# Optimization experiments

Measured on AMD Instinct MI355X. Metric: run time of the kernel, lower is better.

Reference implementation:

```python
import jax, jax.numpy as jnp
import numpy as np
import math

EPS = 1e-5

def layernorm(x, g, b):
    mu = jnp.mean(x, axis=-1, keepdims=True)
    var = jnp.var(x, axis=-1, keepdims=True)
    return (x - mu) * jax.lax.rsqrt(var + EPS) * g + b

def setup_inputs() -> dict:
    key = jax.random.key(0)
    ks = jax.random.split(key, 12)
    B, T, E, H = 4, 2048, 128, 8
    D = H * E          # 1024
    F = 4 * D          # 4096
    s = 0.02
    return {
        "X":     jax.random.normal(ks[0], (B, T, E), jnp.float32),
        "ln1_g": jnp.ones((E,), jnp.float32),
        "ln1_b": jnp.zeros((E,), jnp.float32),
        "Wq":    jax.random.normal(ks[1], (H, E, E), jnp.float32) * s,
        "bq":    jax.random.normal(ks[2], (H, E), jnp.float32) * s,
        "Wk":    jax.random.normal(ks[3], (H, E, E), jnp.float32) * s,
        "bk":    jax.random.normal(ks[4], (H, E), jnp.float32) * s,
        "Wv":    jax.random.normal(ks[5], (H, E, E), jnp.float32) * s,
        "bv":    jax.random.normal(ks[6], (H, E), jnp.float32) * s,
        "ln2_g": jnp.ones((D,), jnp.float32),
        "ln2_b": jnp.zeros((D,), jnp.float32),
        "W1":    jax.random.normal(ks[7], (D, F), jnp.float32) * s,
        "b1":    jax.random.normal(ks[8], (F,), jnp.float32) * s,
        "W2":    jax.random.normal(ks[9], (F, E), jnp.float32) * s,
        "b2":    jax.random.normal(ks[10], (E,), jnp.float32) * s,
    }

def reference(X, ln1_g, ln1_b, Wq, bq, Wk, bk, Wv, bv, ln2_g, ln2_b, W1, b1, W2, b2):
    B, T, E = X.shape
    Xn = layernorm(X, ln1_g, ln1_b)                       # [B,T,E]
    # per-head projections, vectorized over heads
    q = jnp.einsum('bte,hef->bhtf', Xn, Wq) + bq[None, :, None, :]
    k = jnp.einsum('bte,hef->bhtf', Xn, Wk) + bk[None, :, None, :]
    v = jnp.einsum('bte,hef->bhtf', Xn, Wv) + bv[None, :, None, :]
    scores = jnp.einsum('bhtf,bhsf->bhts', q, k) / math.sqrt(E)
    # causal mask: positions with s > t set to -inf (triu offset=1)
    t_idx = jnp.arange(T)
    mask = t_idx[None, :] > t_idx[:, None]                # [T,S], True above diag
    scores = jnp.where(mask[None, None], -jnp.inf, scores)
    # NOTE: original code softmaxes over dim = ndim-2, i.e. the QUERY axis
    attn = jax.nn.softmax(scores, axis=-2)
    out = jnp.einsum('bhts,bhsf->bhtf', attn, v)          # [B,H,T,E]
    # concat heads along last dim (head order preserved)
    concat = jnp.transpose(out, (0, 2, 1, 3)).reshape(B, T, -1)  # [B,T,H*E]
    h = layernorm(concat, ln2_g, ln2_b)
    mid = jax.nn.gelu(h @ W1 + b1, approximate=False)
    return mid @ W2 + b2                                   # [B,T,E]
```

## Files before the change

kernel.cpp:

```cpp
#include <hip/hip_runtime.h>
#include <hip/hip_bf16.h>
#include <math.h>

typedef __hip_bfloat16 bf16;
typedef __attribute__((ext_vector_type(8))) short short8;
typedef __attribute__((ext_vector_type(4))) float floatx4;

#define B_ 4
#define T_ 2048
#define E_ 128
#define H_ 8
#define D_ 1024
#define F_ 4096
#define M_ 8192

static __device__ __forceinline__ float b2f(bf16 v){ return __bfloat162float(v); }
static __device__ __forceinline__ bf16  f2b(float v){ return __float2bfloat16(v); }
static __device__ __forceinline__ short f2bs(float v){ bf16 h = __float2bfloat16(v); return *(short*)&h; }

static __device__ __forceinline__ void glds16(const bf16* g, void* l){
  __builtin_amdgcn_global_load_lds((const __attribute__((address_space(1))) void*)g,
                                   (__attribute__((address_space(3))) void*)l, 16, 0, 0);
}

__global__ void detect_dtype_k(const unsigned int* __restrict__ g, int* __restrict__ flag){
  if (threadIdx.x == 0) flag[0] = (g[0] == 0x3F803F80u) ? 1 : 0;
}

__global__ void convert_misc_k(const void* s0, const void* s1, const void* s2, const void* s3,
                               const void* s4, const void* s5, const void* s6, const void* s7,
                               const void* s8,
                               bf16* g1, bf16* b1, bf16* bqkv, bf16* g2, bf16* b2l,
                               bf16* bb1, bf16* bb2, const int* __restrict__ flag){
  int i = blockIdx.x * 256 + threadIdx.x;
  if (i >= 9600) return;
  int fl = flag[0];
  const void* src; bf16* dst; int off;
  if      (i <  128){ src = s0; dst = g1;          off = i;        }
  else if (i <  256){ src = s1; dst = b1;          off = i - 128;  }
  else if (i < 1280){ src = s2; dst = bqkv;        off = i - 256;  }
  else if (i < 2304){ src = s3; dst = bqkv + 1024; off = i - 1280; }
  else if (i < 3328){ src = s4; dst = bqkv + 2048; off = i - 2304; }
  else if (i < 4352){ src = s5; dst = g2;          off = i - 3328; }
  else if (i < 5376){ src = s6; dst = b2l;         off = i - 4352; }
  else if (i < 9472){ src = s7; dst = bb1;         off = i - 5376; }
  else              { src = s8; dst = bb2;         off = i - 9472; }
  dst[off] = fl ? ((const bf16*)src)[off] : f2b(((const float*)src)[off]);
}

__global__ __launch_bounds__(256) void transpose_cvt_k(const void* __restrict__ src, bf16* __restrict__ dst,
                                                       int R, int C, const int* __restrict__ flag){
  __shared__ float tile[32][33];
  int r0 = blockIdx.y * 32, c0 = blockIdx.x * 32;
  int tx = threadIdx.x & 31, ty = threadIdx.x >> 5;
  int fl = flag[0];
  #pragma unroll
  for (int i = 0; i < 32; i += 8){
    size_t idx = (size_t)(r0 + ty + i) * C + c0 + tx;
    tile[ty + i][tx] = fl ? b2f(((const bf16*)src)[idx]) : ((const float*)src)[idx];
  }
  __syncthreads();
  #pragma unroll
  for (int i = 0; i < 32; i += 8){
    dst[(size_t)(c0 + ty + i) * R + r0 + tx] = f2b(tile[tx][ty + i]);
  }
}

__global__ __launch_bounds__(256) void transpose_qkv_k(const void* __restrict__ Wq, const void* __restrict__ Wk,
                                                       const void* __restrict__ Wv, bf16* __restrict__ dst,
                                                       const int* __restrict__ flag){
  __shared__ float tile[32][33];
  int sel = blockIdx.z >> 3, h = blockIdx.z & 7;
  const void* src = (sel == 0) ? Wq : (sel == 1) ? Wk : Wv;
  size_t mo = (size_t)h * E_ * E_;
  bf16* d = dst + (size_t)sel * H_ * E_ * E_ + mo;
  int r0 = blockIdx.y * 32, c0 = blockIdx.x * 32;
  int tx = threadIdx.x & 31, ty = threadIdx.x >> 5;
  int fl = flag[0];
  #pragma unroll
  for (int i = 0; i < 32; i += 8){
    size_t idx = mo + (size_t)(r0 + ty + i) * E_ + c0 + tx;
    tile[ty + i][tx] = fl ? b2f(((const bf16*)src)[idx]) : ((const float*)src)[idx];
  }
  __syncthreads();
  #pragma unroll
  for (int i = 0; i < 32; i += 8){
    d[(size_t)(c0 + ty + i) * E_ + r0 + tx] = f2b(tile[tx][ty + i]);
  }
}

__global__ __launch_bounds__(256) void ln1_k(const void* __restrict__ X, const bf16* __restrict__ g,
                                             const bf16* __restrict__ b, bf16* __restrict__ out,
                                             const int* __restrict__ flag){
  int row = blockIdx.x * 4 + (threadIdx.x >> 6);
  int lane = threadIdx.x & 63;
  float x0, x1;
  if (flag[0]){
    const bf16* xp = (const bf16*)X + (size_t)row * E_;
    x0 = b2f(xp[lane]); x1 = b2f(xp[lane + 64]);
  } else {
    const float* xp = (const float*)X + (size_t)row * E_;
    x0 = xp[lane]; x1 = xp[lane + 64];
  }
  float s  = x0 + x1;
  float s2 = x0 * x0 + x1 * x1;
  #pragma unroll
  for (int o = 32; o > 0; o >>= 1){ s += __shfl_xor(s, o, 64); s2 += __shfl_xor(s2, o, 64); }
  float mu  = s * (1.0f / 128.0f);
  float var = s2 * (1.0f / 128.0f) - mu * mu;
  float rs  = rsqrtf(var + 1e-5f);
  out[(size_t)row * E_ + lane]      = f2b((x0 - mu) * rs * b2f(g[lane])      + b2f(b[lane]));
  out[(size_t)row * E_ + lane + 64] = f2b((x1 - mu) * rs * b2f(g[lane + 64]) + b2f(b[lane + 64]));
}

template<int EPI>
__global__ __launch_bounds__(256, 3) void gemm_mfma_k(
    const bf16* __restrict__ A, const bf16* __restrict__ Bt,
    const bf16* __restrict__ bias, void* __restrict__ out,
    int K, const int* __restrict__ flag)
{
  __shared__ __align__(16) short As[2][4][128][8];
  __shared__ __align__(16) short Bs[2][4][128][8];
  int tid = threadIdx.x;
  int lane = tid & 63, w = tid >> 6;
  int quad = lane >> 4, l16 = lane & 15;
  int wm = w & 1, wn = w >> 1;
  int m0 = blockIdx.y * 128;
  int n0, nit;
  size_t kstart;
  if (EPI == 3){ n0 = 0; int kc = K >> 3; kstart = (size_t)blockIdx.x * kc; nit = kc >> 5; }
  else         { n0 = blockIdx.x * 128; kstart = 0; nit = K >> 5; }

  int seg0 = w * 2, seg1 = w * 2 + 1;
  int kq0 = seg0 & 3, mb0 = (seg0 >> 2) * 64;
  int kq1 = seg1 & 3, mb1 = (seg1 >> 2) * 64;
  const bf16* pa0 = A  + (size_t)(m0 + mb0 + lane) * K + kstart + kq0 * 8;
  const bf16* pa1 = A  + (size_t)(m0 + mb1 + lane) * K + kstart + kq1 * 8;
  const bf16* pb0 = Bt + (size_t)(n0 + mb0 + lane) * K + kstart + kq0 * 8;
  const bf16* pb1 = Bt + (size_t)(n0 + mb1 + lane) * K + kstart + kq1 * 8;
  uint4 ra0 = *(const uint4*)pa0, ra1 = *(const uint4*)pa1;
  uint4 rb0 = *(const uint4*)pb0, rb1 = *(const uint4*)pb1;

  floatx4 acc[4][4];
  #pragma unroll
  for (int i = 0; i < 4; i++)
    #pragma unroll
    for (int j = 0; j < 4; j++) acc[i][j] = (floatx4){0.f, 0.f, 0.f, 0.f};

  for (int it = 0; it < nit; it++){
    int buf = it & 1;
    *(uint4*)&As[buf][kq0][mb0 + lane][0] = ra0;
    *(uint4*)&As[buf][kq1][mb1 + lane][0] = ra1;
    *(uint4*)&Bs[buf][kq0][mb0 + lane][0] = rb0;
    *(uint4*)&Bs[buf][kq1][mb1 + lane][0] = rb1;
    __syncthreads();
    if (it + 1 < nit){
      int ko = (it + 1) << 5;
      ra0 = *(const uint4*)(pa0 + ko); ra1 = *(const uint4*)(pa1 + ko);
      rb0 = *(const uint4*)(pb0 + ko); rb1 = *(const uint4*)(pb1 + ko);
    }
    short8 af[4], bfr[4];
    #pragma unroll
    for (int i = 0; i < 4; i++) af[i]  = *(const short8*)&As[buf][quad][wm * 64 + i * 16 + l16][0];
    #pragma unroll
    for (int j = 0; j < 4; j++) bfr[j] = *(const short8*)&Bs[buf][quad][wn * 64 + j * 16 + l16][0];
    #pragma unroll
    for (int i = 0; i < 4; i++)
      #pragma unroll
      for (int j = 0; j < 4; j++)
        acc[i][j] = __builtin_amdgcn_mfma_f32_16x16x32_bf16(af[i], bfr[j], acc[i][j], 0, 0, 0);
  }

  bf16* po = (EPI == 3) ? (bf16*)out + (size_t)blockIdx.x * M_ * E_ : nullptr;
  #pragma unroll
  for (int i = 0; i < 4; i++){
    #pragma unroll
    for (int j = 0; j < 4; j++){
      int nn = n0 + wn * 64 + j * 16 + l16;
      float bv = (EPI == 3) ? 0.0f : b2f(bias[nn]);
      if (EPI == 0){
        int sel = nn >> 10, h = (nn >> 7) & 7, f = nn & 127;
        size_t SZ = (size_t)B_ * H_ * T_ * E_;
        int mmb = m0 + wm * 64 + i * 16 + quad * 4;
        int b = mmb >> 11, t = mmb & (T_ - 1);
        if (sel < 2){
          #pragma unroll
          for (int r = 0; r < 4; r++)
            ((bf16*)out)[(size_t)sel * SZ + (((size_t)(b * H_ + h) * T_ + t + r) * E_) + f] =
              f2b(acc[i][j][r] + bv);
        } else {
          ushort4 pk;
          #pragma unroll
          for (int r = 0; r < 4; r++) ((short*)&pk)[r] = f2bs(acc[i][j][r] + bv);
          *(ushort4*)((bf16*)out + 2 * SZ + (((size_t)(b * H_ + h) * E_ + f) * T_) + t) = pk;
        }
      } else {
        #pragma unroll
        for (int r = 0; r < 4; r++){
          int mm = m0 + wm * 64 + i * 16 + quad * 4 + r;
          po[(size_t)mm * E_ + nn] = f2b(acc[i][j][r] + bv);
        }
      }
    }
  }
}

__global__ __launch_bounds__(512, 2) void mlp1_swz_k(
    const bf16* __restrict__ A, const bf16* __restrict__ Bt,
    const bf16* __restrict__ bias, bf16* __restrict__ out)
{
  __shared__ __align__(16) short As[4][256][32];
  __shared__ __align__(16) short Bs[4][256][32];
  constexpr int K  = D_;
  constexpr int NK = K / 32;
  constexpr int BUFB = 256 * 32 * 2;

  int tid = threadIdx.x;
  int lane = tid & 63, w = tid >> 6;
  int quad = lane >> 4, l16 = lane & 15;
  int wm = w & 1, wn = w >> 1;
  int m0 = blockIdx.y * 256, n0 = blockIdx.x * 256;

  int u0 = w * 2, u1 = u0 + 1;
  int rl = lane >> 2;
  int cg = (lane & 3) ^ ((lane >> 3) & 3);
  const bf16* gA0 = A  + (size_t)(m0 + u0 * 16 + rl) * K + cg * 8;
  const bf16* gA1 = A  + (size_t)(m0 + u1 * 16 + rl) * K + cg * 8;
  const bf16* gB0 = Bt + (size_t)(n0 + u0 * 16 + rl) * K + cg * 8;
  const bf16* gB1 = Bt + (size_t)(n0 + u1 * 16 + rl) * K + cg * 8;

  int offA[2][4], offB[4];
  #pragma unroll
  for (int h = 0; h < 2; h++)
    #pragma unroll
    for (int i = 0; i < 4; i++){
      int ra = wm * 128 + h * 64 + i * 16 + l16;
      offA[h][i] = (ra << 6) + ((quad ^ ((ra >> 1) & 3)) << 4);
    }
  #pragma unroll
  for (int j = 0; j < 4; j++){
    int rb = wn * 64 + j * 16 + l16;
    offB[j] = (rb << 6) + ((quad ^ ((rb >> 1) & 3)) << 4);
  }

  #pragma unroll
  for (int t = 0; t < 3; t++){
    int ko = t * 32;
    glds16(gA0 + ko, &As[t][u0 * 16][0]);
    glds16(gA1 + ko, &As[t][u1 * 16][0]);
    glds16(gB0 + ko, &Bs[t][u0 * 16][0]);
    glds16(gB1 + ko, &Bs[t][u1 * 16][0]);
  }
  asm volatile("s_waitcnt vmcnt(8)" ::: "memory");
  __builtin_amdgcn_s_barrier();

  floatx4 acc[2][4][4];
  #pragma unroll
  for (int h = 0; h < 2; h++)
    #pragma unroll
    for (int i = 0; i < 4; i++)
      #pragma unroll
      for (int j = 0; j < 4; j++) acc[h][i][j] = (floatx4){0.f, 0.f, 0.f, 0.f};

  #pragma unroll 1
  for (int k = 0; k < NK; ++k){
    int bk = k & 3, b3 = (k + 3) & 3;
    const char* baseA = (const char*)As + bk * BUFB;
    const char* baseB = (const char*)Bs + bk * BUFB;
    short8 bf8[4], a2[2][4];
    #pragma unroll
    for (int j = 0; j < 4; j++) bf8[j]   = *(const short8*)(baseB + offB[j]);
    #pragma unroll
    for (int i = 0; i < 4; i++) a2[0][i] = *(const short8*)(baseA + offA[0][i]);
    #pragma unroll
    for (int i = 0; i < 4; i++) a2[1][i] = *(const short8*)(baseA + offA[1][i]);
    if (k + 3 < NK){
      int ko = (k + 3) * 32;
      glds16(gA0 + ko, &As[b3][u0 * 16][0]);
      glds16(gA1 + ko, &As[b3][u1 * 16][0]);
      glds16(gB0 + ko, &Bs[b3][u0 * 16][0]);
      glds16(gB1 + ko, &Bs[b3][u1 * 16][0]);
    }
    __builtin_amdgcn_s_setprio(1);
    #pragma unroll
    for (int h = 0; h < 2; h++)
      #pragma unroll
      for (int i = 0; i < 4; i++)
        #pragma unroll
        for (int j = 0; j < 4; j++)
          acc[h][i][j] = __builtin_amdgcn_mfma_f32_16x16x32_bf16(a2[h][i], bf8[j], acc[h][i][j], 0, 0, 0);
    __builtin_amdgcn_s_setprio(0);
    if (k < NK - 3)       { asm volatile("s_waitcnt vmcnt(8)" ::: "memory"); }
    else if (k == NK - 3) { asm volatile("s_waitcnt vmcnt(4)" ::: "memory"); }
    else if (k == NK - 2) { asm volatile("s_waitcnt vmcnt(0)" ::: "memory"); }
    asm volatile("s_waitcnt lgkmcnt(0)" ::: "memory");
    __builtin_amdgcn_sched_barrier(0);
    __builtin_amdgcn_s_barrier();
  }

  #pragma unroll
  for (int h = 0; h < 2; h++){
    #pragma unroll
    for (int i = 0; i < 4; i++){
      #pragma unroll
      for (int j = 0; j < 4; j++){
        int nn = n0 + wn * 64 + j * 16 + l16;
        float bv = b2f(bias[nn]);
        #pragma unroll
        for (int r = 0; r < 4; r++){
          int mm = m0 + wm * 128 + h * 64 + i * 16 + quad * 4 + r;
          float v = acc[h][i][j][r] + bv;
          float e = __expf(1.5957691216057308f * v * (1.0f + 0.044715f * v * v));
          out[(size_t)mm * F_ + nn] = f2b(v - v / (1.0f + e));
        }
      }
    }
  }
}

__global__ __launch_bounds__(256) void mlp2_fin_k(const bf16* __restrict__ P, const bf16* __restrict__ bias,
                                                  void* __restrict__ out, const int* __restrict__ flag){
  int i = blockIdx.x * 256 + threadIdx.x;
  const size_t S = (size_t)M_ * E_;
  float v = b2f(bias[i & (E_ - 1)]);
  #pragma unroll
  for (int k = 0; k < 8; k++) v += b2f(P[i + k * S]);
  if (flag[0]) ((bf16*)out)[i] = f2b(v);
  else         ((float*)out)[i] = v;
}

__global__ __launch_bounds__(256, 2) void colstats_k(const bf16* __restrict__ Q, const bf16* __restrict__ K,
                                                     float* __restrict__ IL){
  __shared__ __align__(16) short Qs[2][4][4][128][8];
  __shared__ float lcol[64];
  const float scale = 0.0883883476483184f;
  int tid = threadIdx.x;
  int lane = tid & 63, w = tid >> 6;
  int quad = lane >> 4, l16 = lane & 15;
  int x = blockIdx.x;
  int c = x & 255, phase = x >> 8;
  int q = c & 7, bh = c >> 3;
  int sblk = (phase == 0) ? q : (phase == 1) ? 31 - q : (phase == 2) ? 8 + q : 23 - q;
  int s0 = sblk * 64;

  short8 bk[4][4];
  #pragma unroll
  for (int j = 0; j < 4; j++)
    #pragma unroll
    for (int kb = 0; kb < 4; kb++)
      bk[j][kb] = *(const short8*)(K + ((size_t)bh * T_ + s0 + j * 16 + l16) * E_ + kb * 32 + quad * 8);

  if (tid < 64) lcol[tid] = 0.0f;

  int t0s = (s0 / 128) * 128;
  int nit = (T_ - t0s) >> 7;

  #pragma unroll
  for (int t2 = 0; t2 < 8; t2++){
    int seg = w * 8 + t2;
    int kb = seg >> 3, kq = (seg >> 1) & 3, hf = seg & 1;
    const bf16* ga = Q + ((size_t)bh * T_ + t0s + hf * 64 + lane) * E_ + kb * 32 + kq * 8;
    __builtin_amdgcn_global_load_lds((const __attribute__((address_space(1))) void*)ga,
                                     (__attribute__((address_space(3))) void*)&Qs[0][kb][kq][hf * 64][0], 16, 0, 0);
  }
  __syncthreads();

  float part[4] = {0.f, 0.f, 0.f, 0.f};
  for (int it = 0; it < nit; it++){
    int buf = it & 1;
    if (it + 1 < nit){
      int nb = buf ^ 1;
      int t1 = t0s + ((it + 1) << 7);
      #pragma unroll
      for (int t2 = 0; t2 < 8; t2++){
        int seg = w * 8 + t2;
        int kb = seg >> 3, kq = (seg >> 1) & 3, hf = seg & 1;
        const bf16* ga = Q + ((size_t)bh * T_ + t1 + hf * 64 + lane) * E_ + kb * 32 + kq * 8;
        __builtin_amdgcn_global_load_lds((const __attribute__((address_space(1))) void*)ga,
                                         (__attribute__((address_space(3))) void*)&Qs[nb][kb][kq][hf * 64][0], 16, 0, 0);
      }
    }
    floatx4 acc[2][4];
    #pragma unroll
    for (int i = 0; i < 2; i++)
      #pragma unroll
      for (int j = 0; j < 4; j++) acc[i][j] = (floatx4){0.f, 0.f, 0.f, 0.f};
    #pragma unroll
    for (int kb = 0; kb < 4; kb++){
      short8 af[2];
      #pragma unroll
      for (int i = 0; i < 2; i++) af[i] = *(const short8*)&Qs[buf][kb][quad][w * 32 + i * 16 + l16][0];
      #pragma unroll
      for (int i = 0; i < 2; i++)
        #pragma unroll
        for (int j = 0; j < 4; j++)
          acc[i][j] = __builtin_amdgcn_mfma_f32_16x16x32_bf16(af[i], bk[j][kb], acc[i][j], 0, 0, 0);
    }
    int t0 = t0s + (it << 7);
    bool dtile = (it == 0);
    #pragma unroll
    for (int i = 0; i < 2; i++)
      #pragma unroll
      for (int j = 0; j < 4; j++)
        #pragma unroll
        for (int r = 0; r < 4; r++){
          float e = __expf(acc[i][j][r] * scale);
          if (dtile){
            int t = t0 + w * 32 + i * 16 + quad * 4 + r;
            int s = s0 + j * 16 + l16;
            if (t < s) e = 0.0f;
          }
          part[j] += e;
        }
    __syncthreads();
  }
  #pragma unroll
  for (int j = 0; j < 4; j++){
    part[j] += __shfl_xor(part[j], 16, 64);
    part[j] += __shfl_xor(part[j], 32, 64);
  }
  if (quad == 0){
    #pragma unroll
    for (int j = 0; j < 4; j++) atomicAdd(&lcol[j * 16 + l16], part[j]);
  }
  __syncthreads();
  if (tid < 64) IL[(size_t)bh * T_ + s0 + tid] = 1.0f / lcol[tid];
}

__global__ __launch_bounds__(256, 2) void attnout_k(const bf16* __restrict__ Q, const bf16* __restrict__ K,
                                                    const bf16* __restrict__ VT, const float* __restrict__ IL,
                                                    bf16* __restrict__ CC){
  __shared__ __align__(16) short Qs[128][136];
  __shared__ __align__(16) short KV[64 * 136 > 128 * 72 ? 64 * 136 : 128 * 72];
  __shared__ __align__(16) short Ps[128][72];
  const float scale = 0.0883883476483184f;
  int tid = threadIdx.x;
  int lane = tid & 63, w = tid >> 6;
  int quad = lane >> 4, l16 = lane & 15;
  int x = blockIdx.x;
  int c = x & 255, phase = x >> 8;
  int q = c & 7, bh = c >> 3;
  int tblk = phase ? (15 - q) : q;
  int t0 = tblk * 128;
  int b = bh >> 3, h = bh & 7;

  #pragma unroll
  for (int i = 0; i < 8; i++){
    int idx = tid + i * 256; int r = idx >> 4, cc = idx & 15;
    *(uint4*)&Qs[r][cc * 8] = *(const uint4*)(Q + ((size_t)bh * T_ + t0 + r) * E_ + cc * 8);
  }
  floatx4 O[2][8];
  #pragma unroll
  for (int i = 0; i < 2; i++)
    #pragma unroll
    for (int n = 0; n < 8; n++) O[i][n] = (floatx4){0.f, 0.f, 0.f, 0.f};

  for (int s0 = 0; s0 < t0 + 128; s0 += 64){
    __syncthreads();
    #pragma unroll
    for (int i = 0; i < 4; i++){
      int idx = tid + i * 256; int r = idx >> 4, cc = idx & 15;
      *(uint4*)&KV[(r) * 136 + cc * 8] = *(const uint4*)(K + ((size_t)bh * T_ + s0 + r) * E_ + cc * 8);
    }
    __syncthreads();
    floatx4 acc[2][4];
    #pragma unroll
    for (int i = 0; i < 2; i++)
      #pragma unroll
      for (int j = 0; j < 4; j++) acc[i][j] = (floatx4){0.f, 0.f, 0.f, 0.f};
    #pragma unroll
    for (int kb = 0; kb < 4; kb++){
      short8 af[2], bfr[4];
      #pragma unroll
      for (int i = 0; i < 2; i++) af[i]  = *(const short8*)&Qs[w * 32 + i * 16 + l16][kb * 32 + quad * 8];
      #pragma unroll
      for (int j = 0; j < 4; j++) bfr[j] = *(const short8*)&KV[(j * 16 + l16) * 136 + kb * 32 + quad * 8];
      #pragma unroll
      for (int i = 0; i < 2; i++)
        #pragma unroll
        for (int j = 0; j < 4; j++)
          acc[i][j] = __builtin_amdgcn_mfma_f32_16x16x32_bf16(af[i], bfr[j], acc[i][j], 0, 0, 0);
    }
    float il[4];
    #pragma unroll
    for (int j = 0; j < 4; j++) il[j] = IL[(size_t)bh * T_ + s0 + j * 16 + l16];
    bool dtile = (s0 + 63 > t0);
    #pragma unroll
    for (int i = 0; i < 2; i++)
      #pragma unroll
      for (int j = 0; j < 4; j++)
        #pragma unroll
        for (int r = 0; r < 4; r++){
          float p = __expf(acc[i][j][r] * scale) * il[j];
          int trow = w * 32 + i * 16 + quad * 4 + r;
          if (dtile){
            int t = t0 + trow, s = s0 + j * 16 + l16;
            if (t < s) p = 0.0f;
          }
          Ps[trow][j * 16 + l16] = f2bs(p);
        }
    __syncthreads();
    #pragma unroll
    for (int i = 0; i < 4; i++){
      int idx = tid + i * 256; int e = idx >> 3, cc = idx & 7;
      *(uint4*)&KV[e * 72 + cc * 8] = *(const uint4*)(VT + ((size_t)bh * E_ + e) * T_ + s0 + cc * 8);
    }
    __syncthreads();
    #pragma unroll
    for (int kb2 = 0; kb2 < 2; kb2++){
      short8 pa[2], vb[8];
      #pragma unroll
      for (int i = 0; i < 2; i++) pa[i] = *(const short8*)&Ps[w * 32 + i * 16 + l16][kb2 * 32 + quad * 8];
      #pragma unroll
      for (int n = 0; n < 8; n++) vb[n] = *(const short8*)&KV[(n * 16 + l16) * 72 + kb2 * 32 + quad * 8];
      #pragma unroll
      for (int i = 0; i < 2; i++)
        #pragma unroll
        for (int n = 0; n < 8; n++)
          O[i][n] = __builtin_amdgcn_mfma_f32_16x16x32_bf16(pa[i], vb[n], O[i][n], 0, 0, 0);
    }
  }
  #pragma unroll
  for (int i = 0; i < 2; i++)
    #pragma unroll
    for (int n = 0; n < 8; n++)
      #pragma unroll
      for (int r = 0; r < 4; r++){
        int t = t0 + w * 32 + i * 16 + quad * 4 + r;
        int e = n * 16 + l16;
        CC[((size_t)(b * T_ + t)) * D_ + h * E_ + e] = f2b(O[i][n][r]);
      }
}

__global__ __launch_bounds__(256) void ln2_k(const bf16* __restrict__ in, const bf16* __restrict__ g,
                                             const bf16* __restrict__ bta, bf16* __restrict__ out){
  __shared__ float wsum[4], wsum2[4];
  int row = blockIdx.x, tid = threadIdx.x;
  const bf16* xp = in + (size_t)row * D_;
  float x[4]; float s = 0.0f, s2 = 0.0f;
  #pragma unroll
  for (int i = 0; i < 4; i++){ x[i] = b2f(xp[tid + i * 256]); s += x[i]; s2 += x[i] * x[i]; }
  #pragma unroll
  for (int o = 32; o > 0; o >>= 1){ s += __shfl_xor(s, o, 64); s2 += __shfl_xor(s2, o, 64); }
  int wid = tid >> 6;
  if ((tid & 63) == 0){ wsum[wid] = s; wsum2[wid] = s2; }
  __syncthreads();
  s  = wsum[0] + wsum[1] + wsum[2] + wsum[3];
  s2 = wsum2[0] + wsum2[1] + wsum2[2] + wsum2[3];
  float mu  = s * (1.0f / 1024.0f);
  float var = s2 * (1.0f / 1024.0f) - mu * mu;
  float rs  = rsqrtf(var + 1e-5f);
  #pragma unroll
  for (int i = 0; i < 4; i++){
    int c = tid + i * 256;
    out[(size_t)row * D_ + c] = f2b((x[i] - mu) * rs * b2f(g[c]) + b2f(bta[c]));
  }
}

static constexpr size_t A256(size_t x){ return (x + 255) & ~(size_t)255; }

extern "C" void kernel_launch(void* const* d_in, const int* in_sizes, int n_in,
                              void* d_out, int out_size, void* d_ws, size_t ws_size,
                              hipStream_t stream){
  (void)in_sizes; (void)n_in; (void)out_size; (void)ws_size;
  char* ws = (char*)d_ws;

  constexpr size_t o_flag  = 0;
  constexpr size_t o_g1    = 256;
  constexpr size_t o_b1    = A256(o_g1    + (size_t)E_ * 2);
  constexpr size_t o_WqkvT = A256(o_b1    + (size_t)E_ * 2);
  constexpr size_t o_bqkv  = A256(o_WqkvT + (size_t)3 * H_ * E_ * E_ * 2);
  constexpr size_t o_g2    = A256(o_bqkv  + (size_t)3 * H_ * E_ * 2);
  constexpr size_t o_b2l   = A256(o_g2    + (size_t)D_ * 2);
  constexpr size_t o_W1T   = A256(o_b2l   + (size_t)D_ * 2);
  constexpr size_t o_bb1   = A256(o_W1T   + (size_t)D_ * F_ * 2);
  constexpr size_t o_W2T   = A256(o_bb1   + (size_t)F_ * 2);
  constexpr size_t o_bb2   = A256(o_W2T   + (size_t)F_ * E_ * 2);
  constexpr size_t o_xn    = A256(o_bb2   + (size_t)E_ * 2);
  constexpr size_t o_q     = A256(o_xn    + (size_t)M_ * E_ * 2);
  constexpr size_t o_k     = o_q + (size_t)B_ * H_ * T_ * E_ * 2;
  constexpr size_t o_vt    = o_k + (size_t)B_ * H_ * T_ * E_ * 2;
  constexpr size_t o_il    = A256(o_vt + (size_t)B_ * H_ * T_ * E_ * 2);
  constexpr size_t o_cc    = A256(o_il + (size_t)B_ * H_ * T_ * 4);
  constexpr size_t o_h2    = A256(o_cc + (size_t)M_ * D_ * 2);
  constexpr size_t o_mid   = o_q;
  constexpr size_t o_part  = o_h2;
  static_assert(o_mid + (size_t)M_ * F_ * 2 <= o_h2, "mid overlaps live h2 buffer");
  static_assert((size_t)8 * M_ * E_ * 2 <= (size_t)M_ * D_ * 2, "partials exceed h2 region");

  int*  flag  = (int*)(ws + o_flag);
  bf16* g1    = (bf16*)(ws + o_g1);
  bf16* b1p   = (bf16*)(ws + o_b1);
  bf16* WqkvT = (bf16*)(ws + o_WqkvT);
  bf16* bqkv  = (bf16*)(ws + o_bqkv);
  bf16* g2    = (bf16*)(ws + o_g2);
  bf16* b2l   = (bf16*)(ws + o_b2l);
  bf16* W1T   = (bf16*)(ws + o_W1T);
  bf16* bb1   = (bf16*)(ws + o_bb1);
  bf16* W2T   = (bf16*)(ws + o_W2T);
  bf16* bb2   = (bf16*)(ws + o_bb2);
  bf16* xn    = (bf16*)(ws + o_xn);
  bf16* Qb    = (bf16*)(ws + o_q);
  bf16* Kb    = (bf16*)(ws + o_k);
  bf16* VTb   = (bf16*)(ws + o_vt);
  float* ILp  = (float*)(ws + o_il);
  bf16* ccp   = (bf16*)(ws + o_cc);
  bf16* h2p   = (bf16*)(ws + o_h2);
  bf16* midp  = (bf16*)(ws + o_mid);
  bf16* part  = (bf16*)(ws + o_part);

  detect_dtype_k<<<1, 64, 0, stream>>>((const unsigned int*)d_in[1], flag);

  convert_misc_k<<<38, 256, 0, stream>>>(d_in[1], d_in[2], d_in[4], d_in[6], d_in[8],
                                         d_in[9], d_in[10], d_in[12], d_in[14],
                                         g1, b1p, bqkv, g2, b2l, bb1, bb2, flag);

  transpose_qkv_k<<<dim3(4, 4, 24), 256, 0, stream>>>(d_in[3], d_in[5], d_in[7], WqkvT, flag);
  transpose_cvt_k<<<dim3(F_ / 32, D_ / 32), 256, 0, stream>>>(d_in[11], W1T, D_, F_, flag);
  transpose_cvt_k<<<dim3(E_ / 32, F_ / 32), 256, 0, stream>>>(d_in[13], W2T, F_, E_, flag);

  ln1_k<<<M_ / 4, 256, 0, stream>>>(d_in[0], g1, b1p, xn, flag);

  gemm_mfma_k<0><<<dim3(3 * D_ / 128, M_ / 128), 256, 0, stream>>>(xn, WqkvT, bqkv, Qb, E_, flag);

  colstats_k<<<1024, 256, 0, stream>>>(Qb, Kb, ILp);
  attnout_k<<<512, 256, 0, stream>>>(Qb, Kb, VTb, ILp, ccp);

  ln2_k<<<M_, 256, 0, stream>>>(ccp, g2, b2l, h2p);

  mlp1_swz_k<<<dim3(F_ / 256, M_ / 256), 512, 0, stream>>>(h2p, W1T, bb1, midp);
  gemm_mfma_k<3><<<dim3(8, M_ / 128), 256, 0, stream>>>(midp, W2T, bb2, part, F_, flag);
  mlp2_fin_k<<<M_ * E_ / 256, 256, 0, stream>>>(part, bb2, d_out, flag);
}
```

Before: 403.2 us.

## Use 4 waves with 128x128 warp tiles in MLP1 GEMM

Restructures the MLP1 GEMM block from 8 waves (each owning a 128x64 tile) to 4 waves, each owning a 128x128 tile with 64 accumulators. Each wave now loads 8 A and 8 B fragments per k-step to feed 64 MFMAs, which raises the ratio of MFMAs to LDS reads. The global-to-LDS prefetch is also moved ahead of the LDS reads, and the setprio hints are removed. The cost is 256 accumulator registers per lane and only one block per CU (launch bounds 256,1), so there are fewer waves available to hide latency, and register pressure or spills become a risk.

```diff
diff --git a/kernel.cpp b/kernel.cpp
--- a/kernel.cpp
+++ b/kernel.cpp
@@ -205,7 +205,7 @@
   }
 }
 
-__global__ __launch_bounds__(512, 2) void mlp1_swz_k(
+__global__ __launch_bounds__(256, 1) void mlp1_w128_k(
     const bf16* __restrict__ A, const bf16* __restrict__ Bt,
     const bf16* __restrict__ bias, bf16* __restrict__ out)
 {
@@ -221,77 +221,68 @@
   int wm = w & 1, wn = w >> 1;
   int m0 = blockIdx.y * 256, n0 = blockIdx.x * 256;
 
-  int u0 = w * 2, u1 = u0 + 1;
   int rl = lane >> 2;
   int cg = (lane & 3) ^ ((lane >> 3) & 3);
-  const bf16* gA0 = A  + (size_t)(m0 + u0 * 16 + rl) * K + cg * 8;
-  const bf16* gA1 = A  + (size_t)(m0 + u1 * 16 + rl) * K + cg * 8;
-  const bf16* gB0 = Bt + (size_t)(n0 + u0 * 16 + rl) * K + cg * 8;
-  const bf16* gB1 = Bt + (size_t)(n0 + u1 * 16 + rl) * K + cg * 8;
-
-  int offA[2][4], offB[4];
-  #pragma unroll
-  for (int h = 0; h < 2; h++)
-    #pragma unroll
-    for (int i = 0; i < 4; i++){
-      int ra = wm * 128 + h * 64 + i * 16 + l16;
-      offA[h][i] = (ra << 6) + ((quad ^ ((ra >> 1) & 3)) << 4);
-    }
-  #pragma unroll
-  for (int j = 0; j < 4; j++){
-    int rb = wn * 64 + j * 16 + l16;
-    offB[j] = (rb << 6) + ((quad ^ ((rb >> 1) & 3)) << 4);
+  const bf16* gA[4]; const bf16* gB[4];
+  #pragma unroll
+  for (int u = 0; u < 4; u++){
+    int uu = w * 4 + u;
+    gA[u] = A  + (size_t)(m0 + uu * 16 + rl) * K + cg * 8;
+    gB[u] = Bt + (size_t)(n0 + uu * 16 + rl) * K + cg * 8;
+  }
+
+  int offA[8], offB[8];
+  #pragma unroll
+  for (int i = 0; i < 8; i++){
+    int ra = wm * 128 + i * 16 + l16;
+    offA[i] = (ra << 6) + ((quad ^ ((ra >> 1) & 3)) << 4);
+    int rb = wn * 128 + i * 16 + l16;
+    offB[i] = (rb << 6) + ((quad ^ ((rb >> 1) & 3)) << 4);
   }
 
   #pragma unroll
   for (int t = 0; t < 3; t++){
     int ko = t * 32;
-    glds16(gA0 + ko, &As[t][u0 * 16][0]);
-    glds16(gA1 + ko, &As[t][u1 * 16][0]);
-    glds16(gB0 + ko, &Bs[t][u0 * 16][0]);
-    glds16(gB1 + ko, &Bs[t][u1 * 16][0]);
-  }
-  asm volatile("s_waitcnt vmcnt(8)" ::: "memory");
+    #pragma unroll
+    for (int u = 0; u < 4; u++){
+      glds16(gA[u] + ko, &As[t][(w * 4 + u) * 16][0]);
+      glds16(gB[u] + ko, &Bs[t][(w * 4 + u) * 16][0]);
+    }
+  }
+  asm volatile("s_waitcnt vmcnt(16)" ::: "memory");
   __builtin_amdgcn_s_barrier();
 
-  floatx4 acc[2][4][4];
-  #pragma unroll
-  for (int h = 0; h < 2; h++)
-    #pragma unroll
-    for (int i = 0; i < 4; i++)
-      #pragma unroll
-      for (int j = 0; j < 4; j++) acc[h][i][j] = (floatx4){0.f, 0.f, 0.f, 0.f};
+  floatx4 acc[8][8];
+  #pragma unroll
+  for (int i = 0; i < 8; i++)
+    #pragma unroll
+    for (int j = 0; j < 8; j++) acc[i][j] = (floatx4){0.f, 0.f, 0.f, 0.f};
 
   #pragma unroll 1
   for (int k = 0; k < NK; ++k){
     int bk = k & 3, b3 = (k + 3) & 3;
+    if (k + 3 < NK){
+      int ko = (k + 3) * 32;
+      #pragma unroll
+      for (int u = 0; u < 4; u++){
+        glds16(gA[u] + ko, &As[b3][(w * 4 + u) * 16][0]);
+        glds16(gB[u] + ko, &Bs[b3][(w * 4 + u) * 16][0]);
+      }
+    }
     const char* baseA = (const char*)As + bk * BUFB;
     const char* baseB = (const char*)Bs + bk * BUFB;
-    short8 bf8[4], a2[2][4];
-    #pragma unroll
-    for (int j = 0; j < 4; j++) bf8[j]   = *(const short8*)(baseB + offB[j]);
-    #pragma unroll
-    for (int i = 0; i < 4; i++) a2[0][i] = *(const short8*)(baseA + offA[0][i]);
-    #pragma unroll
-    for (int i = 0; i < 4; i++) a2[1][i] = *(const short8*)(baseA + offA[1][i]);
-    if (k + 3 < NK){
-      int ko = (k + 3) * 32;
-      glds16(gA0 + ko, &As[b3][u0 * 16][0]);
-      glds16(gA1 + ko, &As[b3][u1 * 16][0]);
-      glds16(gB0 + ko, &Bs[b3][u0 * 16][0]);
-      glds16(gB1 + ko, &Bs[b3][u1 * 16][0]);
-    }
-    __builtin_amdgcn_s_setprio(1);
-    #pragma unroll
-    for (int h = 0; h < 2; h++)
-      #pragma unroll
-      for (int i = 0; i < 4; i++)
-        #pragma unroll
-        for (int j = 0; j < 4; j++)
-          acc[h][i][j] = __builtin_amdgcn_mfma_f32_16x16x32_bf16(a2[h][i], bf8[j], acc[h][i][j], 0, 0, 0);
-    __builtin_amdgcn_s_setprio(0);
-    if (k < NK - 3)       { asm volatile("s_waitcnt vmcnt(8)" ::: "memory"); }
-    else if (k == NK - 3) { asm volatile("s_waitcnt vmcnt(4)" ::: "memory"); }
+    short8 a2[8];
+    #pragma unroll
+    for (int i = 0; i < 8; i++) a2[i] = *(const short8*)(baseA + offA[i]);
+    #pragma unroll
+    for (int j = 0; j < 8; j++){
+      short8 bf = *(const short8*)(baseB + offB[j]);
+      #pragma unroll
+      for (int i = 0; i < 8; i++)
+        acc[i][j] = __builtin_amdgcn_mfma_f32_16x16x32_bf16(a2[i], bf, acc[i][j], 0, 0, 0);
+    }
+    if (k < NK - 3)       { asm volatile("s_waitcnt vmcnt(16)" ::: "memory"); }
+    else if (k == NK - 3) { asm volatile("s_waitcnt vmcnt(8)" ::: "memory"); }
     else if (k == NK - 2) { asm volatile("s_waitcnt vmcnt(0)" ::: "memory"); }
     asm volatile("s_waitcnt lgkmcnt(0)" ::: "memory");
     __builtin_amdgcn_sched_barrier(0);
@@ -299,20 +290,17 @@
   }
 
   #pragma unroll
-  for (int h = 0; h < 2; h++){
-    #pragma unroll
-    for (int i = 0; i < 4; i++){
-      #pragma unroll
-      for (int j = 0; j < 4; j++){
-        int nn = n0 + wn * 64 + j * 16 + l16;
-        float bv = b2f(bias[nn]);
-        #pragma unroll
-        for (int r = 0; r < 4; r++){
-          int mm = m0 + wm * 128 + h * 64 + i * 16 + quad * 4 + r;
-          float v = acc[h][i][j][r] + bv;
-          float e = __expf(1.5957691216057308f * v * (1.0f + 0.044715f * v * v));
-          out[(size_t)mm * F_ + nn] = f2b(v - v / (1.0f + e));
-        }
+  for (int i = 0; i < 8; i++){
+    #pragma unroll
+    for (int j = 0; j < 8; j++){
+      int nn = n0 + wn * 128 + j * 16 + l16;
+      float bv = b2f(bias[nn]);
+      #pragma unroll
+      for (int r = 0; r < 4; r++){
+        int mm = m0 + wm * 128 + i * 16 + quad * 4 + r;
+        float v = acc[i][j][r] + bv;
+        float e = __expf(1.5957691216057308f * v * (1.0f + 0.044715f * v * v));
+        out[(size_t)mm * F_ + nn] = f2b(v - v / (1.0f + e));
       }
     }
   }
@@ -628,7 +616,7 @@
 
   ln2_k<<<M_, 256, 0, stream>>>(ccp, g2, b2l, h2p);
 
-  mlp1_swz_k<<<dim3(F_ / 256, M_ / 256), 512, 0, stream>>>(h2p, W1T, bb1, midp);
+  mlp1_w128_k<<<dim3(F_ / 256, M_ / 256), 256, 0, stream>>>(h2p, W1T, bb1, midp);
   gemm_mfma_k<3><<<dim3(8, M_ / 128), 256, 0, stream>>>(midp, W2T, bb2, part, F_, flag);
   mlp2_fin_k<<<M_ * E_ / 256, 256, 0, stream>>>(part, bb2, d_out, flag);
 }
```

New measurement: 493.9 us. +22.5%, slower.

## Prefetch K/V tiles through registers and transpose S MFMA for packed P stores

Applied to the files above, without the earlier changes.

The attention-output kernel now loads the next K tile and the current V^T tile into registers ahead of time, so global loads overlap with the MFMA and softmax work instead of stalling right before each shared-memory write. The score MFMA swaps its operands (K times Q) so each lane holds four consecutive key columns and can write P to shared memory as one packed 4-element store instead of scalar stores. The inverse column sums are staged once per tile through shared memory. In exchange the kernel holds more registers (Kreg/Vreg plus index arrays), which may pressure the 2-blocks-per-CU occupancy target.

```diff
diff --git a/kernel.cpp b/kernel.cpp
--- a/kernel.cpp
+++ b/kernel.cpp
@@ -433,6 +433,7 @@
   __shared__ __align__(16) short Qs[128][136];
   __shared__ __align__(16) short KV[64 * 136 > 128 * 72 ? 64 * 136 : 128 * 72];
   __shared__ __align__(16) short Ps[128][72];
+  __shared__ float lil[64];
   const float scale = 0.0883883476483184f;
   int tid = threadIdx.x;
   int lane = tid & 63, w = tid >> 6;
@@ -455,55 +456,76 @@
     #pragma unroll
     for (int n = 0; n < 8; n++) O[i][n] = (floatx4){0.f, 0.f, 0.f, 0.f};
 
+  int kr[4], kc[4], ve[4], vc[4];
+  #pragma unroll
+  for (int i = 0; i < 4; i++){
+    int idx = tid + i * 256;
+    kr[i] = idx >> 4; kc[i] = idx & 15;
+    ve[i] = idx >> 3; vc[i] = idx & 7;
+  }
+  uint4 Kreg[4], Vreg[4];
+  #pragma unroll
+  for (int i = 0; i < 4; i++)
+    Kreg[i] = *(const uint4*)(K + ((size_t)bh * T_ + kr[i]) * E_ + kc[i] * 8);
+
   for (int s0 = 0; s0 < t0 + 128; s0 += 64){
     __syncthreads();
     #pragma unroll
-    for (int i = 0; i < 4; i++){
-      int idx = tid + i * 256; int r = idx >> 4, cc = idx & 15;
-      *(uint4*)&KV[(r) * 136 + cc * 8] = *(const uint4*)(K + ((size_t)bh * T_ + s0 + r) * E_ + cc * 8);
-    }
+    for (int i = 0; i < 4; i++)
+      *(uint4*)&KV[kr[i] * 136 + kc[i] * 8] = Kreg[i];
+    if (tid < 64) lil[tid] = IL[(size_t)bh * T_ + s0 + tid];
+    #pragma unroll
+    for (int i = 0; i < 4; i++)
+      Vreg[i] = *(const uint4*)(VT + ((size_t)bh * E_ + ve[i]) * T_ + s0 + vc[i] * 8);
     __syncthreads();
-    floatx4 acc[2][4];
-    #pragma unroll
-    for (int i = 0; i < 2; i++)
-      #pragma unroll
-      for (int j = 0; j < 4; j++) acc[i][j] = (floatx4){0.f, 0.f, 0.f, 0.f};
+    floatx4 acc[4][2];
+    #pragma unroll
+    for (int j = 0; j < 4; j++)
+      #pragma unroll
+      for (int i = 0; i < 2; i++) acc[j][i] = (floatx4){0.f, 0.f, 0.f, 0.f};
     #pragma unroll
     for (int kb = 0; kb < 4; kb++){
-      short8 af[2], bfr[4];
-      #pragma unroll
-      for (int i = 0; i < 2; i++) af[i]  = *(const short8*)&Qs[w * 32 + i * 16 + l16][kb * 32 + quad * 8];
-      #pragma unroll
-      for (int j = 0; j < 4; j++) bfr[j] = *(const short8*)&KV[(j * 16 + l16) * 136 + kb * 32 + quad * 8];
-      #pragma unroll
-      for (int i = 0; i < 2; i++)
-        #pragma unroll
-        for (int j = 0; j < 4; j++)
-          acc[i][j] = __builtin_amdgcn_mfma_f32_16x16x32_bf16(af[i], bfr[j], acc[i][j], 0, 0, 0);
-    }
-    float il[4];
-    #pragma unroll
-    for (int j = 0; j < 4; j++) il[j] = IL[(size_t)bh * T_ + s0 + j * 16 + l16];
+      short8 kf[4], qf[2];
+      #pragma unroll
+      for (int j = 0; j < 4; j++) kf[j] = *(const short8*)&KV[(j * 16 + l16) * 136 + kb * 32 + quad * 8];
+      #pragma unroll
+      for (int i = 0; i < 2; i++) qf[i] = *(const short8*)&Qs[w * 32 + i * 16 + l16][kb * 32 + quad * 8];
+      #pragma unroll
+      for (int j = 0; j < 4; j++)
+        #pragma unroll
+        for (int i = 0; i < 2; i++)
+          acc[j][i] = __builtin_amdgcn_mfma_f32_16x16x32_bf16(kf[j], qf[i], acc[j][i], 0, 0, 0);
+    }
+    floatx4 il4[4];
+    #pragma unroll
+    for (int j = 0; j < 4; j++) il4[j] = *(const floatx4*)&lil[j * 16 + quad * 4];
     bool dtile = (s0 + 63 > t0);
     #pragma unroll
-    for (int i = 0; i < 2; i++)
-      #pragma unroll
-      for (int j = 0; j < 4; j++)
+    for (int i = 0; i < 2; i++){
+      int trow = w * 32 + i * 16 + l16;
+      #pragma unroll
+      for (int j = 0; j < 4; j++){
+        ushort4 pk;
         #pragma unroll
         for (int r = 0; r < 4; r++){
-          float p = __expf(acc[i][j][r] * scale) * il[j];
-          int trow = w * 32 + i * 16 + quad * 4 + r;
+          float p = __expf(acc[j][i][r] * scale) * il4[j][r];
           if (dtile){
-            int t = t0 + trow, s = s0 + j * 16 + l16;
+            int t = t0 + trow, s = s0 + j * 16 + quad * 4 + r;
             if (t < s) p = 0.0f;
           }
-          Ps[trow][j * 16 + l16] = f2bs(p);
+          ((short*)&pk)[r] = f2bs(p);
         }
+        *(ushort4*)&Ps[trow][j * 16 + quad * 4] = pk;
+      }
+    }
     __syncthreads();
     #pragma unroll
-    for (int i = 0; i < 4; i++){
-      int idx = tid + i * 256; int e = idx >> 3, cc = idx & 7;
-      *(uint4*)&KV[e * 72 + cc * 8] = *(const uint4*)(VT + ((size_t)bh * E_ + e) * T_ + s0 + cc * 8);
+    for (int i = 0; i < 4; i++)
+      *(uint4*)&KV[ve[i] * 72 + vc[i] * 8] = Vreg[i];
+    if (s0 + 64 < t0 + 128){
+      #pragma unroll
+      for (int i = 0; i < 4; i++)
+        Kreg[i] = *(const uint4*)(K + ((size_t)bh * T_ + s0 + 64 + kr[i]) * E_ + kc[i] * 8);
     }
     __syncthreads();
     #pragma unroll
```

Measured after the change: 447.2 us. 10.9% more time.
